# Kernel tuning notes

Hardware: AMD Instinct MI355X
Metric: run time of the kernel (lower is better)

The kernel has to match this reference:

```python
import math
import jax, jax.numpy as jnp
import numpy as np

D_MODEL = 1024
HEADS = 16
D_K = D_MODEL // HEADS
B, S = 8, 1024


def setup_inputs() -> dict:
    key = jax.random.key(0)
    ks = jax.random.split(key, 12)
    s = 1.0 / math.sqrt(D_MODEL)
    return {
        "values": jax.random.normal(ks[0], (B, S, D_MODEL), jnp.float32),
        "keys": jax.random.normal(ks[1], (B, S, D_MODEL), jnp.float32),
        "query": jax.random.normal(ks[2], (B, S, D_MODEL), jnp.float32),
        "mask": jnp.ones((B, 1, 1, S), jnp.int32),
        "Wq": jax.random.normal(ks[3], (D_MODEL, D_MODEL), jnp.float32) * s,
        "bq": jnp.zeros((D_MODEL,), jnp.float32),
        "Wk": jax.random.normal(ks[4], (D_MODEL, D_MODEL), jnp.float32) * s,
        "bk": jnp.zeros((D_MODEL,), jnp.float32),
        "Wv": jax.random.normal(ks[5], (D_MODEL, D_MODEL), jnp.float32) * s,
        "bv": jnp.zeros((D_MODEL,), jnp.float32),
        "Wo": jax.random.normal(ks[6], (D_MODEL, D_MODEL), jnp.float32) * s,
        "bo": jnp.zeros((D_MODEL,), jnp.float32),
    }


def reference(values, keys, query, mask, Wq, bq, Wk, bk, Wv, bv, Wo, bo):
    b, qlen, d = query.shape
    vlen, klen = values.shape[1], keys.shape[1]
    # projections (torch Linear math: x @ W + b with W stored [in, out])
    v = (values @ Wv + bv).reshape(b, vlen, HEADS, D_K)
    k = (keys @ Wk + bk).reshape(b, klen, HEADS, D_K)
    q = (query @ Wq + bq).reshape(b, qlen, HEADS, D_K)
    # full [b, h, q, k] scores (faithful to the non-flash original)
    energy = jnp.einsum('nqhd,nkhd->nhqk', q, k)
    energy = jnp.where(mask == 0, jnp.float32(-1e20), energy)
    # NOTE: original scales by sqrt(d_model), not sqrt(d_k)
    attn = jax.nn.softmax(energy / math.sqrt(D_MODEL), axis=3)
    out = jnp.einsum('nhql,nlhd->nqhd', attn, v).reshape(b, qlen, d)
    return out @ Wo + bo
```

## Files before the change

kernel.cpp:

```cpp
#include <hip/hip_runtime.h>

#define DM     1024
#define NHEADS 16
#define DK     64
#define NB     8
#define SEQ    1024
#define MROWS  (NB * SEQ)
#define NQ     ((size_t)MROWS * DM)

typedef unsigned short u16;
typedef __attribute__((ext_vector_type(8))) __bf16 bf16x8;
typedef __attribute__((ext_vector_type(8))) short  short8v;
typedef __attribute__((ext_vector_type(4))) float  f32x4;

typedef const __attribute__((address_space(1))) void* gas_ptr;
typedef __attribute__((address_space(3))) void*       las_ptr;

__device__ __forceinline__ void load_lds16(const void* g, void* l) {
    __builtin_amdgcn_global_load_lds((gas_ptr)g, (las_ptr)l, 16, 0, 0);
}
__device__ __forceinline__ void load_lds4(const void* g, void* l) {
    __builtin_amdgcn_global_load_lds((gas_ptr)g, (las_ptr)l, 4, 0, 0);
}

__device__ __forceinline__ u16 bf16_rne(float x) {
    unsigned int u = __float_as_uint(x);
    u += 0x7FFFu + ((u >> 16) & 1u);
    return (u16)(u >> 16);
}

__global__ __launch_bounds__(256)
void conv_split(const float* __restrict__ in, u16* __restrict__ hi,
                u16* __restrict__ lo)
{
    size_t i8 = ((size_t)blockIdx.x * 256 + threadIdx.x) * 8;
    float4 x0 = *(const float4*)(in + i8);
    float4 x1 = *(const float4*)(in + i8 + 4);
    float xs[8] = {x0.x, x0.y, x0.z, x0.w, x1.x, x1.y, x1.z, x1.w};
    short8v vh, vl;
#pragma unroll
    for (int j = 0; j < 8; ++j) {
        u16 h = bf16_rne(xs[j]);
        float hf = __uint_as_float((unsigned int)h << 16);
        vh[j] = (short)h;
        vl[j] = (short)bf16_rne(xs[j] - hf);
    }
    *(short8v*)(hi + i8) = vh;
    *(short8v*)(lo + i8) = vl;
}

__global__ __launch_bounds__(256)
void conv_w(const float* __restrict__ W0, const float* __restrict__ W1,
            const float* __restrict__ W2, const float* __restrict__ W3,
            u16* __restrict__ hiB, u16* __restrict__ loB)
{
    __shared__ float Wf[32][68];
    const int t = threadIdx.x;
    const int n0 = blockIdx.x * 64, k0 = blockIdx.y * 32, z = blockIdx.z;
    const float* W = (z == 0) ? W0 : (z == 1) ? W1 : (z == 2) ? W2 : W3;
    u16* hi = hiB + (size_t)z * DM * DM;
    u16* lo = loB + (size_t)z * DM * DM;

#pragma unroll
    for (int p = 0; p < 2; ++p) {
        int fid = p * 256 + t;
        int kk = fid >> 4, c4 = fid & 15;
        *(float4*)&Wf[kk][c4 * 4] =
            *(const float4*)(W + (size_t)(k0 + kk) * DM + n0 + c4 * 4);
    }
    __syncthreads();

    const int n = t >> 2, g = t & 3;
    short8v vh, vl;
#pragma unroll
    for (int j = 0; j < 8; ++j) {
        float x = Wf[g * 8 + j][n];
        u16 h = bf16_rne(x);
        float hf = __uint_as_float((unsigned int)h << 16);
        vh[j] = (short)h;
        vl[j] = (short)bf16_rne(x - hf);
    }
    size_t off = (size_t)(n0 + n) * DM + k0 + g * 8;
    *(short8v*)(hi + off) = vh;
    *(short8v*)(lo + off) = vl;
}

template <int MODE>
__global__ __launch_bounds__(256)
void gemm_split_t(const u16* __restrict__ Agh, const u16* __restrict__ Agl,
                  const u16* __restrict__ Bgh, const u16* __restrict__ Bgl,
                  const float* __restrict__ bias, float* __restrict__ Cf,
                  u16* __restrict__ C1, u16* __restrict__ C2)
{
    __shared__ __align__(16) u16 Ah[128 * 32], Al[128 * 32],
                                 Bh[128 * 32], Bl[128 * 32];
    const int t = threadIdx.x, lane = t & 63, wid = t >> 6;
    const int m0 = blockIdx.x * 128, n0 = blockIdx.y * 128;
    const int wm0 = (wid >> 1) * 64, wn0 = (wid & 1) * 64;
    const int ln = lane & 15, blk = lane >> 4;

    const u16* gsrc = (wid == 0) ? Agh : (wid == 1) ? Agl
                    : (wid == 2) ? Bgh : Bgl;
    u16* ldst = (wid == 0) ? Ah : (wid == 1) ? Al : (wid == 2) ? Bh : Bl;
    const int r0 = (wid < 2) ? m0 : n0;
    const int lr = lane >> 2, sl = lane & 3;
    const int gg = sl ^ ((lr >> 1) & 3);
    const u16* gbase = gsrc + (size_t)(r0 + lr) * DM + gg * 8;

    f32x4 zero4 = {0.f, 0.f, 0.f, 0.f};
    f32x4 acc[4][4];
#pragma unroll
    for (int i = 0; i < 4; ++i)
#pragma unroll
        for (int j = 0; j < 4; ++j) acc[i][j] = zero4;

    for (int kt = 0; kt < 1024; kt += 32) {
        __syncthreads();
#pragma unroll
        for (int i = 0; i < 8; ++i)
            load_lds16(gbase + (size_t)i * 16 * DM + kt, ldst + i * 512);
        __syncthreads();

        bf16x8 bfh[4], bfl[4];
#pragma unroll
        for (int bn = 0; bn < 4; ++bn) {
            int rn = wn0 + bn * 16 + ln;
            int off = rn * 32 + ((blk ^ ((rn >> 1) & 3)) << 3);
            bfh[bn] = *(const bf16x8*)(Bh + off);
            bfl[bn] = *(const bf16x8*)(Bl + off);
        }
#pragma unroll
        for (int am = 0; am < 4; ++am) {
            int rm = wm0 + am * 16 + ln;
            int off = rm * 32 + ((blk ^ ((rm >> 1) & 3)) << 3);
            bf16x8 afh = *(const bf16x8*)(Ah + off);
            bf16x8 afl = *(const bf16x8*)(Al + off);
#pragma unroll
            for (int bn = 0; bn < 4; ++bn) {
                acc[am][bn] = __builtin_amdgcn_mfma_f32_16x16x32_bf16(
                    afh, bfh[bn], acc[am][bn], 0, 0, 0);
                acc[am][bn] = __builtin_amdgcn_mfma_f32_16x16x32_bf16(
                    afh, bfl[bn], acc[am][bn], 0, 0, 0);
                acc[am][bn] = __builtin_amdgcn_mfma_f32_16x16x32_bf16(
                    afl, bfh[bn], acc[am][bn], 0, 0, 0);
            }
        }
    }

#pragma unroll
    for (int bn = 0; bn < 4; ++bn) {
        int col = n0 + wn0 + bn * 16 + ln;
        float bs = bias[col];
#pragma unroll
        for (int am = 0; am < 4; ++am) {
#pragma unroll
            for (int r = 0; r < 4; ++r) {
                int row = m0 + wm0 + am * 16 + blk * 4 + r;
                float v = acc[am][bn][r] + bs;
                size_t idx = (size_t)row * DM + col;
                if (MODE == 0) {
                    Cf[idx] = v;
                } else if (MODE == 1) {
                    u16 h = bf16_rne(v);
                    float hf = __uint_as_float((unsigned int)h << 16);
                    C1[idx] = h;
                    C2[idx] = bf16_rne(v - hf);
                } else {
                    C1[idx] = bf16_rne(v);
                }
            }
        }
    }
}

__global__ __launch_bounds__(256)
void v_transpose(const u16* __restrict__ Vbf, u16* __restrict__ Vt)
{
    __shared__ u16 Ls[64][66];
    const int t = threadIdx.x;
    const int s0 = blockIdx.x * 64, h = blockIdx.y, b = blockIdx.z;
#pragma unroll
    for (int p = 0; p < 2; ++p) {
        int id = p * 256 + t;
        int s = id >> 3, c8 = id & 7;
        short8v v = *(const short8v*)(Vbf + (size_t)(b * SEQ + s0 + s) * DM +
                                      h * DK + c8 * 8);
#pragma unroll
        for (int j = 0; j < 8; ++j) Ls[s][c8 * 8 + j] = (u16)v[j];
    }
    __syncthreads();
#pragma unroll
    for (int p = 0; p < 2; ++p) {
        int id = p * 256 + t;
        int d = id >> 3, s8 = id & 7;
        short8v v;
#pragma unroll
        for (int j = 0; j < 8; ++j) v[j] = (short)Ls[s8 * 8 + j][d];
        *(short8v*)(Vt + (size_t)((b * NHEADS + h) * DK + d) * SEQ + s0 +
                    s8 * 8) = v;
    }
}

__global__ __launch_bounds__(256)
void attn_mfma(const u16* __restrict__ Qh, const u16* __restrict__ Ql,
               const u16* __restrict__ Kh, const u16* __restrict__ Kl,
               const u16* __restrict__ Vt, const int* __restrict__ mask,
               float* __restrict__ OutA)
{
    __shared__ __align__(16) u16 Qhs[128 * 64], Qls[128 * 64];
    __shared__ __align__(16) u16 Khs[64 * 64], Kls[64 * 64], Vts[64 * 64];
    __shared__ __align__(16) u16 Ps[4][16 * 64];
    __shared__ int msk_s[64];

    const int t = threadIdx.x, lane = t & 63, wid = t >> 6;
    const int q0 = blockIdx.x * 128;
    const int h = blockIdx.y, b = blockIdx.z;
    const int ln = lane & 15, blk = lane >> 4;

    const int srow = lane >> 3;
    const int schk = (lane & 7) ^ srow;

    {
        const size_t qg =
            (size_t)(b * SEQ + q0 + srow) * DM + h * DK + schk * 8;
        for (int i = wid; i < 16; i += 4) {
            load_lds16(Qh + qg + (size_t)i * 8 * DM, (char*)Qhs + i * 1024);
            load_lds16(Ql + qg + (size_t)i * 8 * DM, (char*)Qls + i * 1024);
        }
    }

    float m_i[2][4], l_i[2][4];
    f32x4 oacc[2][4];
    f32x4 zero4 = {0.f, 0.f, 0.f, 0.f};
#pragma unroll
    for (int am = 0; am < 2; ++am) {
#pragma unroll
        for (int r = 0; r < 4; ++r) { m_i[am][r] = -INFINITY; l_i[am][r] = 0.f; }
#pragma unroll
        for (int bn = 0; bn < 4; ++bn) oacc[am][bn] = zero4;
    }

    for (int kv0 = 0; kv0 < SEQ; kv0 += 64) {
        __syncthreads();
        if (wid == 0) {
            const size_t kg =
                (size_t)(b * SEQ + kv0 + srow) * DM + h * DK + schk * 8;
#pragma unroll
            for (int i = 0; i < 8; ++i)
                load_lds16(Kh + kg + (size_t)i * 8 * DM, (char*)Khs + i * 1024);
        } else if (wid == 1) {
            const size_t kg =
                (size_t)(b * SEQ + kv0 + srow) * DM + h * DK + schk * 8;
#pragma unroll
            for (int i = 0; i < 8; ++i)
                load_lds16(Kl + kg + (size_t)i * 8 * DM, (char*)Kls + i * 1024);
        } else if (wid == 2) {
            const size_t vg =
                (size_t)((b * NHEADS + h) * DK + srow) * SEQ + kv0 + schk * 8;
#pragma unroll
            for (int i = 0; i < 8; ++i)
                load_lds16(Vt + vg + (size_t)i * 8 * SEQ, (char*)Vts + i * 1024);
        } else {
            load_lds4(mask + (size_t)b * SEQ + kv0 + lane, (char*)msk_s);
        }
        __syncthreads();

        int mvals[4];
#pragma unroll
        for (int ct = 0; ct < 4; ++ct) mvals[ct] = msk_s[ct * 16 + ln];

#pragma unroll
        for (int am = 0; am < 2; ++am) {
            const int qrow = wid * 32 + am * 16 + ln;
            bf16x8 qh[2], ql[2];
#pragma unroll
            for (int ks = 0; ks < 2; ++ks) {
                int idx = qrow * 64 + (((ks * 4 + blk) ^ (qrow & 7)) << 3);
                qh[ks] = *(const bf16x8*)(Qhs + idx);
                ql[ks] = *(const bf16x8*)(Qls + idx);
            }
            f32x4 s[4];
#pragma unroll
            for (int ct = 0; ct < 4; ++ct) s[ct] = zero4;
#pragma unroll
            for (int ct = 0; ct < 4; ++ct) {
                int krow = ct * 16 + ln;
#pragma unroll
                for (int ks = 0; ks < 2; ++ks) {
                    int idx = krow * 64 + (((ks * 4 + blk) ^ (krow & 7)) << 3);
                    bf16x8 kf = *(const bf16x8*)(Khs + idx);
                    bf16x8 kg2 = *(const bf16x8*)(Kls + idx);
                    s[ct] = __builtin_amdgcn_mfma_f32_16x16x32_bf16(
                        qh[ks], kf, s[ct], 0, 0, 0);
                    s[ct] = __builtin_amdgcn_mfma_f32_16x16x32_bf16(
                        qh[ks], kg2, s[ct], 0, 0, 0);
                    s[ct] = __builtin_amdgcn_mfma_f32_16x16x32_bf16(
                        ql[ks], kf, s[ct], 0, 0, 0);
                }
            }
#pragma unroll
            for (int ct = 0; ct < 4; ++ct) {
                const bool mz = (mvals[ct] == 0);
#pragma unroll
                for (int r = 0; r < 4; ++r) {
                    float e = mz ? -1e20f : s[ct][r];
                    s[ct][r] = e * 0.03125f;
                }
            }
#pragma unroll
            for (int r = 0; r < 4; ++r) {
                float mt = fmaxf(fmaxf(s[0][r], s[1][r]),
                                 fmaxf(s[2][r], s[3][r]));
#pragma unroll
                for (int off = 1; off < 16; off <<= 1)
                    mt = fmaxf(mt, __shfl_xor(mt, off, 16));
                float mn = fmaxf(m_i[am][r], mt);
                float al = __expf(m_i[am][r] - mn);
                m_i[am][r] = mn;
                float rs = 0.f;
#pragma unroll
                for (int ct = 0; ct < 4; ++ct) {
                    float p = __expf(s[ct][r] - mn);
                    s[ct][r] = p;
                    rs += p;
                }
#pragma unroll
                for (int off = 1; off < 16; off <<= 1)
                    rs += __shfl_xor(rs, off, 16);
                l_i[am][r] = l_i[am][r] * al + rs;
#pragma unroll
                for (int bn = 0; bn < 4; ++bn) oacc[am][bn][r] *= al;
            }
            u16* P = &Ps[wid][0];
#pragma unroll
            for (int ct = 0; ct < 4; ++ct) {
                int slot = ct * 2 + (ln >> 3);
#pragma unroll
                for (int r = 0; r < 4; ++r) {
                    int q = blk * 4 + r;
                    P[q * 64 + ((slot ^ (q & 7)) << 3) + (ln & 7)] =
                        bf16_rne(s[ct][r]);
                }
            }
#pragma unroll
            for (int ks = 0; ks < 2; ++ks) {
                int pidx = ln * 64 + (((ks * 4 + blk) ^ (ln & 7)) << 3);
                bf16x8 pa = *(const bf16x8*)(P + pidx);
#pragma unroll
                for (int bn = 0; bn < 4; ++bn) {
                    int vrow = bn * 16 + ln;
                    int vidx =
                        vrow * 64 + (((ks * 4 + blk) ^ (vrow & 7)) << 3);
                    bf16x8 vb = *(const bf16x8*)(Vts + vidx);
                    oacc[am][bn] = __builtin_amdgcn_mfma_f32_16x16x32_bf16(
                        pa, vb, oacc[am][bn], 0, 0, 0);
                }
            }
        }
    }

#pragma unroll
    for (int am = 0; am < 2; ++am) {
#pragma unroll
        for (int r = 0; r < 4; ++r) {
            int q = q0 + wid * 32 + am * 16 + blk * 4 + r;
            float inv = 1.f / l_i[am][r];
#pragma unroll
            for (int bn = 0; bn < 4; ++bn) {
                OutA[(size_t)(b * SEQ + q) * DM + h * DK + bn * 16 + ln] =
                    oacc[am][bn][r] * inv;
            }
        }
    }
}

extern "C" void kernel_launch(void* const* d_in, const int* in_sizes, int n_in,
                              void* d_out, int out_size, void* d_ws, size_t ws_size,
                              hipStream_t stream)
{
    const float* values = (const float*)d_in[0];
    const float* keys   = (const float*)d_in[1];
    const float* query  = (const float*)d_in[2];
    const int*   mask   = (const int*)d_in[3];
    const float* Wq = (const float*)d_in[4];
    const float* bq = (const float*)d_in[5];
    const float* Wk = (const float*)d_in[6];
    const float* bk = (const float*)d_in[7];
    const float* Wv = (const float*)d_in[8];
    const float* bv = (const float*)d_in[9];
    const float* Wo = (const float*)d_in[10];
    const float* bo = (const float*)d_in[11];
    float* out = (float*)d_out;

    u16* Qh   = (u16*)d_ws;
    u16* Ql   = Qh + NQ;
    u16* Kh   = Ql + NQ;
    u16* Kl   = Kh + NQ;
    u16* Vbf  = Kl + NQ;
    u16* Vtb  = Vbf + NQ;
    u16* Wthi = Vtb + NQ;
    u16* Wtlo = Wthi + (size_t)4 * DM * DM;
    u16* tAhi = Wtlo + (size_t)4 * DM * DM;
    u16* tAlo = tAhi + NQ;
    float* Ao = (float*)tAhi;
    u16* AoHi = Vbf;
    u16* AoLo = Vtb;

    const u16* WqH = Wthi + 0 * (size_t)DM * DM;
    const u16* WkH = Wthi + 1 * (size_t)DM * DM;
    const u16* WvH = Wthi + 2 * (size_t)DM * DM;
    const u16* WoH = Wthi + 3 * (size_t)DM * DM;
    const u16* WqL = Wtlo + 0 * (size_t)DM * DM;
    const u16* WkL = Wtlo + 1 * (size_t)DM * DM;
    const u16* WvL = Wtlo + 2 * (size_t)DM * DM;
    const u16* WoL = Wtlo + 3 * (size_t)DM * DM;

    dim3 blk(256);
    const int convGrid = (int)(NQ / 2048);
    const dim3 gemmGrid(MROWS / 128, DM / 128, 1);

    conv_w<<<dim3(16, 32, 4), blk, 0, stream>>>(Wq, Wk, Wv, Wo, Wthi, Wtlo);

    conv_split<<<convGrid, blk, 0, stream>>>(query, tAhi, tAlo);
    gemm_split_t<1><<<gemmGrid, blk, 0, stream>>>(tAhi, tAlo, WqH, WqL, bq,
                                                  nullptr, Qh, Ql);
    conv_split<<<convGrid, blk, 0, stream>>>(keys, tAhi, tAlo);
    gemm_split_t<1><<<gemmGrid, blk, 0, stream>>>(tAhi, tAlo, WkH, WkL, bk,
                                                  nullptr, Kh, Kl);
    conv_split<<<convGrid, blk, 0, stream>>>(values, tAhi, tAlo);
    gemm_split_t<2><<<gemmGrid, blk, 0, stream>>>(tAhi, tAlo, WvH, WvL, bv,
                                                  nullptr, Vbf, nullptr);
    v_transpose<<<dim3(16, NHEADS, NB), blk, 0, stream>>>(Vbf, Vtb);

    attn_mfma<<<dim3(SEQ / 128, NHEADS, NB), blk, 0, stream>>>(
        Qh, Ql, Kh, Kl, Vtb, mask, Ao);

    conv_split<<<convGrid, blk, 0, stream>>>(Ao, AoHi, AoLo);
    gemm_split_t<0><<<gemmGrid, blk, 0, stream>>>(AoHi, AoLo, WoH, WoL, bo,
                                                  out, nullptr, nullptr);
}
```

Before: 559.2 us.

## Batch QKV conversion and projections, fuse output split into attention, lazy softmax rescale

Merges the three input conversions and the three QKV projection GEMMs into single launches over a z-dimension, when the workspace is large enough. The attention kernel now writes the hi/lo bf16 split of its output directly, which removes the fp32 round trip and a separate conversion pass. Q fragments are kept in registers instead of LDS. Softmax rescaling is skipped unless the running max grows by more than a threshold, and the scale is folded into an fma. The GEMM mode becomes a runtime argument, which may add branching in the epilogue, and the lazy-max threshold risks exp overflow margins.

```diff
diff --git a/kernel.cpp b/kernel.cpp
--- a/kernel.cpp
+++ b/kernel.cpp
@@ -29,11 +29,10 @@
     return (u16)(u >> 16);
 }
 
-__global__ __launch_bounds__(256)
-void conv_split(const float* __restrict__ in, u16* __restrict__ hi,
-                u16* __restrict__ lo)
-{
-    size_t i8 = ((size_t)blockIdx.x * 256 + threadIdx.x) * 8;
+__device__ __forceinline__ void split_store8(const float* __restrict__ in,
+                                             u16* __restrict__ hi,
+                                             u16* __restrict__ lo, size_t i8)
+{
     float4 x0 = *(const float4*)(in + i8);
     float4 x1 = *(const float4*)(in + i8 + 4);
     float xs[8] = {x0.x, x0.y, x0.z, x0.w, x1.x, x1.y, x1.z, x1.w};
@@ -47,6 +46,28 @@
     }
     *(short8v*)(hi + i8) = vh;
     *(short8v*)(lo + i8) = vl;
+}
+
+__global__ __launch_bounds__(256)
+void conv_split(const float* __restrict__ in, u16* __restrict__ hi,
+                u16* __restrict__ lo)
+{
+    size_t i8 = ((size_t)blockIdx.x * 256 + threadIdx.x) * 8;
+    split_store8(in, hi, lo, i8);
+}
+
+__global__ __launch_bounds__(256)
+void conv_qkv(const float* __restrict__ q, const float* __restrict__ k,
+              const float* __restrict__ v, u16* __restrict__ qh,
+              u16* __restrict__ ql, u16* __restrict__ kh, u16* __restrict__ kl,
+              u16* __restrict__ vh, u16* __restrict__ vl)
+{
+    const int z = blockIdx.z;
+    const float* in = (z == 0) ? q : (z == 1) ? k : v;
+    u16* hi = (z == 0) ? qh : (z == 1) ? kh : vh;
+    u16* lo = (z == 0) ? ql : (z == 1) ? kl : vl;
+    size_t i8 = ((size_t)blockIdx.x * 256 + threadIdx.x) * 8;
+    split_store8(in, hi, lo, i8);
 }
 
 __global__ __launch_bounds__(256)
@@ -85,12 +106,11 @@
     *(short8v*)(lo + off) = vl;
 }
 
-template <int MODE>
-__global__ __launch_bounds__(256)
-void gemm_split_t(const u16* __restrict__ Agh, const u16* __restrict__ Agl,
-                  const u16* __restrict__ Bgh, const u16* __restrict__ Bgl,
-                  const float* __restrict__ bias, float* __restrict__ Cf,
-                  u16* __restrict__ C1, u16* __restrict__ C2)
+__device__ __forceinline__ void gemm_body(
+    const u16* __restrict__ Agh, const u16* __restrict__ Agl,
+    const u16* __restrict__ Bgh, const u16* __restrict__ Bgl,
+    const float* __restrict__ bias, int mode, float* __restrict__ Cf,
+    u16* __restrict__ C1, u16* __restrict__ C2)
 {
     __shared__ __align__(16) u16 Ah[128 * 32], Al[128 * 32],
                                  Bh[128 * 32], Bl[128 * 32];
@@ -158,9 +178,9 @@
                 int row = m0 + wm0 + am * 16 + blk * 4 + r;
                 float v = acc[am][bn][r] + bs;
                 size_t idx = (size_t)row * DM + col;
-                if (MODE == 0) {
+                if (mode == 0) {
                     Cf[idx] = v;
-                } else if (MODE == 1) {
+                } else if (mode == 1) {
                     u16 h = bf16_rne(v);
                     float hf = __uint_as_float((unsigned int)h << 16);
                     C1[idx] = h;
@@ -174,6 +194,38 @@
 }
 
 __global__ __launch_bounds__(256)
+void gemm_one(const u16* __restrict__ Agh, const u16* __restrict__ Agl,
+              const u16* __restrict__ Bgh, const u16* __restrict__ Bgl,
+              const float* __restrict__ bias, int mode, float* __restrict__ Cf,
+              u16* __restrict__ C1, u16* __restrict__ C2)
+{
+    gemm_body(Agh, Agl, Bgh, Bgl, bias, mode, Cf, C1, C2);
+}
+
+__global__ __launch_bounds__(256)
+void gemm_qkv(const u16* __restrict__ Aqh, const u16* __restrict__ Aql,
+              const u16* __restrict__ Akh, const u16* __restrict__ Akl,
+              const u16* __restrict__ Avh, const u16* __restrict__ Avl,
+              const u16* __restrict__ Wqh, const u16* __restrict__ Wql,
+              const u16* __restrict__ Wkh, const u16* __restrict__ Wkl,
+              const u16* __restrict__ Wvh, const u16* __restrict__ Wvl,
+              const float* __restrict__ bq, const float* __restrict__ bk,
+              const float* __restrict__ bv, u16* __restrict__ Qh,
+              u16* __restrict__ Ql, u16* __restrict__ Kh, u16* __restrict__ Kl,
+              u16* __restrict__ Vbf)
+{
+    const int z = blockIdx.z;
+    const u16* Ah = (z == 0) ? Aqh : (z == 1) ? Akh : Avh;
+    const u16* Al = (z == 0) ? Aql : (z == 1) ? Akl : Avl;
+    const u16* Bh = (z == 0) ? Wqh : (z == 1) ? Wkh : Wvh;
+    const u16* Bl = (z == 0) ? Wql : (z == 1) ? Wkl : Wvl;
+    const float* bias = (z == 0) ? bq : (z == 1) ? bk : bv;
+    u16* C1 = (z == 0) ? Qh : (z == 1) ? Kh : Vbf;
+    u16* C2 = (z == 0) ? Ql : (z == 1) ? Kl : nullptr;
+    gemm_body(Ah, Al, Bh, Bl, bias, (z == 2) ? 2 : 1, nullptr, C1, C2);
+}
+
+__global__ __launch_bounds__(256)
 void v_transpose(const u16* __restrict__ Vbf, u16* __restrict__ Vt)
 {
     __shared__ u16 Ls[64][66];
@@ -205,9 +257,8 @@
 void attn_mfma(const u16* __restrict__ Qh, const u16* __restrict__ Ql,
                const u16* __restrict__ Kh, const u16* __restrict__ Kl,
                const u16* __restrict__ Vt, const int* __restrict__ mask,
-               float* __restrict__ OutA)
-{
-    __shared__ __align__(16) u16 Qhs[128 * 64], Qls[128 * 64];
+               u16* __restrict__ AoHi, u16* __restrict__ AoLo)
+{
     __shared__ __align__(16) u16 Khs[64 * 64], Kls[64 * 64], Vts[64 * 64];
     __shared__ __align__(16) u16 Ps[4][16 * 64];
     __shared__ int msk_s[64];
@@ -216,16 +267,18 @@
     const int q0 = blockIdx.x * 128;
     const int h = blockIdx.y, b = blockIdx.z;
     const int ln = lane & 15, blk = lane >> 4;
-
     const int srow = lane >> 3;
     const int schk = (lane & 7) ^ srow;
 
-    {
-        const size_t qg =
-            (size_t)(b * SEQ + q0 + srow) * DM + h * DK + schk * 8;
-        for (int i = wid; i < 16; i += 4) {
-            load_lds16(Qh + qg + (size_t)i * 8 * DM, (char*)Qhs + i * 1024);
-            load_lds16(Ql + qg + (size_t)i * 8 * DM, (char*)Qls + i * 1024);
+    bf16x8 qfh[2][2], qfl[2][2];
+#pragma unroll
+    for (int am = 0; am < 2; ++am) {
+        int row = q0 + wid * 32 + am * 16 + ln;
+        size_t base = (size_t)(b * SEQ + row) * DM + h * DK;
+#pragma unroll
+        for (int ks = 0; ks < 2; ++ks) {
+            qfh[am][ks] = *(const bf16x8*)(Qh + base + (ks * 4 + blk) * 8);
+            qfl[am][ks] = *(const bf16x8*)(Ql + base + (ks * 4 + blk) * 8);
         }
     }
 
@@ -271,14 +324,6 @@
 
 #pragma unroll
         for (int am = 0; am < 2; ++am) {
-            const int qrow = wid * 32 + am * 16 + ln;
-            bf16x8 qh[2], ql[2];
-#pragma unroll
-            for (int ks = 0; ks < 2; ++ks) {
-                int idx = qrow * 64 + (((ks * 4 + blk) ^ (qrow & 7)) << 3);
-                qh[ks] = *(const bf16x8*)(Qhs + idx);
-                ql[ks] = *(const bf16x8*)(Qls + idx);
-            }
             f32x4 s[4];
 #pragma unroll
             for (int ct = 0; ct < 4; ++ct) s[ct] = zero4;
@@ -291,20 +336,18 @@
                     bf16x8 kf = *(const bf16x8*)(Khs + idx);
                     bf16x8 kg2 = *(const bf16x8*)(Kls + idx);
                     s[ct] = __builtin_amdgcn_mfma_f32_16x16x32_bf16(
-                        qh[ks], kf, s[ct], 0, 0, 0);
+                        qfh[am][ks], kf, s[ct], 0, 0, 0);
                     s[ct] = __builtin_amdgcn_mfma_f32_16x16x32_bf16(
-                        qh[ks], kg2, s[ct], 0, 0, 0);
+                        qfh[am][ks], kg2, s[ct], 0, 0, 0);
                     s[ct] = __builtin_amdgcn_mfma_f32_16x16x32_bf16(
-                        ql[ks], kf, s[ct], 0, 0, 0);
+                        qfl[am][ks], kf, s[ct], 0, 0, 0);
                 }
             }
 #pragma unroll
             for (int ct = 0; ct < 4; ++ct) {
-                const bool mz = (mvals[ct] == 0);
-#pragma unroll
-                for (int r = 0; r < 4; ++r) {
-                    float e = mz ? -1e20f : s[ct][r];
-                    s[ct][r] = e * 0.03125f;
+                if (mvals[ct] == 0) {
+#pragma unroll
+                    for (int r = 0; r < 4; ++r) s[ct][r] = -1e20f;
                 }
             }
 #pragma unroll
@@ -314,22 +357,26 @@
 #pragma unroll
                 for (int off = 1; off < 16; off <<= 1)
                     mt = fmaxf(mt, __shfl_xor(mt, off, 16));
-                float mn = fmaxf(m_i[am][r], mt);
-                float al = __expf(m_i[am][r] - mn);
-                m_i[am][r] = mn;
+                float pmax = mt * 0.03125f;
+                if (pmax > m_i[am][r] + 8.f) {
+                    float al = __expf(m_i[am][r] - pmax);
+                    m_i[am][r] = pmax;
+                    l_i[am][r] *= al;
+#pragma unroll
+                    for (int bn = 0; bn < 4; ++bn) oacc[am][bn][r] *= al;
+                }
+                float mn = m_i[am][r];
                 float rs = 0.f;
 #pragma unroll
                 for (int ct = 0; ct < 4; ++ct) {
-                    float p = __expf(s[ct][r] - mn);
+                    float p = __expf(fmaf(s[ct][r], 0.03125f, -mn));
                     s[ct][r] = p;
                     rs += p;
                 }
 #pragma unroll
                 for (int off = 1; off < 16; off <<= 1)
                     rs += __shfl_xor(rs, off, 16);
-                l_i[am][r] = l_i[am][r] * al + rs;
-#pragma unroll
-                for (int bn = 0; bn < 4; ++bn) oacc[am][bn][r] *= al;
+                l_i[am][r] += rs;
             }
             u16* P = &Ps[wid][0];
 #pragma unroll
@@ -365,10 +412,15 @@
         for (int r = 0; r < 4; ++r) {
             int q = q0 + wid * 32 + am * 16 + blk * 4 + r;
             float inv = 1.f / l_i[am][r];
+            size_t rowbase = (size_t)(b * SEQ + q) * DM + h * DK;
 #pragma unroll
             for (int bn = 0; bn < 4; ++bn) {
-                OutA[(size_t)(b * SEQ + q) * DM + h * DK + bn * 16 + ln] =
-                    oacc[am][bn][r] * inv;
+                float v = oacc[am][bn][r] * inv;
+                u16 uh = bf16_rne(v);
+                float hf = __uint_as_float((unsigned int)uh << 16);
+                size_t idx = rowbase + bn * 16 + ln;
+                AoHi[idx] = uh;
+                AoLo[idx] = bf16_rne(v - hf);
             }
         }
     }
@@ -392,50 +444,88 @@
     const float* bo = (const float*)d_in[11];
     float* out = (float*)d_out;
 
-    u16* Qh   = (u16*)d_ws;
-    u16* Ql   = Qh + NQ;
-    u16* Kh   = Ql + NQ;
-    u16* Kl   = Kh + NQ;
-    u16* Vbf  = Kl + NQ;
-    u16* Vtb  = Vbf + NQ;
-    u16* Wthi = Vtb + NQ;
-    u16* Wtlo = Wthi + (size_t)4 * DM * DM;
-    u16* tAhi = Wtlo + (size_t)4 * DM * DM;
-    u16* tAlo = tAhi + NQ;
-    float* Ao = (float*)tAhi;
-    u16* AoHi = Vbf;
-    u16* AoLo = Vtb;
-
-    const u16* WqH = Wthi + 0 * (size_t)DM * DM;
-    const u16* WkH = Wthi + 1 * (size_t)DM * DM;
-    const u16* WvH = Wthi + 2 * (size_t)DM * DM;
-    const u16* WoH = Wthi + 3 * (size_t)DM * DM;
-    const u16* WqL = Wtlo + 0 * (size_t)DM * DM;
-    const u16* WkL = Wtlo + 1 * (size_t)DM * DM;
-    const u16* WvL = Wtlo + 2 * (size_t)DM * DM;
-    const u16* WoL = Wtlo + 3 * (size_t)DM * DM;
-
     dim3 blk(256);
     const int convGrid = (int)(NQ / 2048);
     const dim3 gemmGrid(MROWS / 128, DM / 128, 1);
-
-    conv_w<<<dim3(16, 32, 4), blk, 0, stream>>>(Wq, Wk, Wv, Wo, Wthi, Wtlo);
-
-    conv_split<<<convGrid, blk, 0, stream>>>(query, tAhi, tAlo);
-    gemm_split_t<1><<<gemmGrid, blk, 0, stream>>>(tAhi, tAlo, WqH, WqL, bq,
-                                                  nullptr, Qh, Ql);
-    conv_split<<<convGrid, blk, 0, stream>>>(keys, tAhi, tAlo);
-    gemm_split_t<1><<<gemmGrid, blk, 0, stream>>>(tAhi, tAlo, WkH, WkL, bk,
-                                                  nullptr, Kh, Kl);
-    conv_split<<<convGrid, blk, 0, stream>>>(values, tAhi, tAlo);
-    gemm_split_t<2><<<gemmGrid, blk, 0, stream>>>(tAhi, tAlo, WvH, WvL, bv,
-                                                  nullptr, Vbf, nullptr);
-    v_transpose<<<dim3(16, NHEADS, NB), blk, 0, stream>>>(Vbf, Vtb);
-
-    attn_mfma<<<dim3(SEQ / 128, NHEADS, NB), blk, 0, stream>>>(
-        Qh, Ql, Kh, Kl, Vtb, mask, Ao);
-
-    conv_split<<<convGrid, blk, 0, stream>>>(Ao, AoHi, AoLo);
-    gemm_split_t<0><<<gemmGrid, blk, 0, stream>>>(AoHi, AoLo, WoH, WoL, bo,
-                                                  out, nullptr, nullptr);
-}
+    const dim3 gemmGrid3(MROWS / 128, DM / 128, 3);
+
+    const bool fused = ws_size >= (size_t)12 * NQ * 2;
+
+    if (fused) {
+        u16* Qh   = (u16*)d_ws;
+        u16* Ql   = Qh + NQ;
+        u16* Kh   = Ql + NQ;
+        u16* Kl   = Kh + NQ;
+        u16* Vbf  = Kl + NQ;
+        u16* Wthi = Vbf + NQ;
+        u16* Wtlo = Wthi + (size_t)4 * DM * DM;
+        u16* tAqh = Wtlo + (size_t)4 * DM * DM;
+        u16* tAql = tAqh + NQ;
+        u16* tAkh = tAql + NQ;
+        u16* tAkl = tAkh + NQ;
+        u16* tAvh = tAkl + NQ;
+        u16* tAvl = tAvh + NQ;
+        u16* Vtb  = tAqh;
+        u16* AoHi = tAkh;
+        u16* AoLo = tAkl;
+
+        const u16* WqH = Wthi + 0 * (size_t)DM * DM;
+        const u16* WkH = Wthi + 1 * (size_t)DM * DM;
+        const u16* WvH = Wthi + 2 * (size_t)DM * DM;
+        const u16* WoH = Wthi + 3 * (size_t)DM * DM;
+        const u16* WqL = Wtlo + 0 * (size_t)DM * DM;
+        const u16* WkL = Wtlo + 1 * (size_t)DM * DM;
+        const u16* WvL = Wtlo + 2 * (size_t)DM * DM;
+        const u16* WoL = Wtlo + 3 * (size_t)DM * DM;
+
+        conv_w<<<dim3(16, 32, 4), blk, 0, stream>>>(Wq, Wk, Wv, Wo, Wthi, Wtlo);
+        conv_qkv<<<dim3(convGrid, 1, 3), blk, 0, stream>>>(
+            query, keys, values, tAqh, tAql, tAkh, tAkl, tAvh, tAvl);
+        gemm_qkv<<<gemmGrid3, blk, 0, stream>>>(
+            tAqh, tAql, tAkh, tAkl, tAvh, tAvl, WqH, WqL, WkH, WkL, WvH, WvL,
+            bq, bk, bv, Qh, Ql, Kh, Kl, Vbf);
+        v_transpose<<<dim3(16, NHEADS, NB), blk, 0, stream>>>(Vbf, Vtb);
+        attn_mfma<<<dim3(SEQ / 128, NHEADS, NB), blk, 0, stream>>>(
+            Qh, Ql, Kh, Kl, Vtb, mask, AoHi, AoLo);
+        gemm_one<<<gemmGrid, blk, 0, stream>>>(AoHi, AoLo, WoH, WoL, bo, 0,
+                                               out, nullptr, nullptr);
+    } else {
+        u16* Qh   = (u16*)d_ws;
+        u16* Ql   = Qh + NQ;
+        u16* Kh   = Ql + NQ;
+        u16* Kl   = Kh + NQ;
+        u16* Vbf  = Kl + NQ;
+        u16* Vtb  = Vbf + NQ;
+        u16* Wthi = Vtb + NQ;
+        u16* Wtlo = Wthi + (size_t)4 * DM * DM;
+        u16* tAhi = Wtlo + (size_t)4 * DM * DM;
+        u16* tAlo = tAhi + NQ;
+        u16* AoHi = tAhi;
+        u16* AoLo = tAlo;
+
+        const u16* WqH = Wthi + 0 * (size_t)DM * DM;
+        const u16* WkH = Wthi + 1 * (size_t)DM * DM;
+        const u16* WvH = Wthi + 2 * (size_t)DM * DM;
+        const u16* WoH = Wthi + 3 * (size_t)DM * DM;
+        const u16* WqL = Wtlo + 0 * (size_t)DM * DM;
+        const u16* WkL = Wtlo + 1 * (size_t)DM * DM;
+        const u16* WvL = Wtlo + 2 * (size_t)DM * DM;
+        const u16* WoL = Wtlo + 3 * (size_t)DM * DM;
+
+        conv_w<<<dim3(16, 32, 4), blk, 0, stream>>>(Wq, Wk, Wv, Wo, Wthi, Wtlo);
+        conv_split<<<convGrid, blk, 0, stream>>>(query, tAhi, tAlo);
+        gemm_one<<<gemmGrid, blk, 0, stream>>>(tAhi, tAlo, WqH, WqL, bq, 1,
+                                               nullptr, Qh, Ql);
+        conv_split<<<convGrid, blk, 0, stream>>>(keys, tAhi, tAlo);
+        gemm_one<<<gemmGrid, blk, 0, stream>>>(tAhi, tAlo, WkH, WkL, bk, 1,
+                                               nullptr, Kh, Kl);
+        conv_split<<<convGrid, blk, 0, stream>>>(values, tAhi, tAlo);
+        gemm_one<<<gemmGrid, blk, 0, stream>>>(tAhi, tAlo, WvH, WvL, bv, 2,
+                                               nullptr, Vbf, nullptr);
+        v_transpose<<<dim3(16, NHEADS, NB), blk, 0, stream>>>(Vbf, Vtb);
+        attn_mfma<<<dim3(SEQ / 128, NHEADS, NB), blk, 0, stream>>>(
+            Qh, Ql, Kh, Kl, Vtb, mask, AoHi, AoLo);
+        gemm_one<<<gemmGrid, blk, 0, stream>>>(AoHi, AoLo, WoH, WoL, bo, 0,
+                                               out, nullptr, nullptr);
+    }
+}
```

After: 556.2 us. About the same (-0.5%).

## Switch to fp16 split precision, fuse QKV GEMMs and V transpose, lazy softmax rescale

Applied to the files above, without the earlier changes.

Replaces the bf16 hi/lo three-MFMA split with fp16, where activations are a single fp16 and only the weights (and Q) keep a hi/lo pair, cutting MFMA count and conversion traffic. The three input casts and the three projection GEMMs each become one launch batched over z. The V transpose is folded into the GEMM epilogue through LDS, and outputs are written with coalesced LDS-staged stores. Attention keeps Q in registers, uses single-precision K, applies a lazy max rescale with a threshold of 8, and writes its output in fp16 so the separate cast before the output GEMM goes away. fp16 range and the reduced split precision put accuracy at risk.

```diff
diff --git a/kernel.cpp b/kernel.cpp
--- a/kernel.cpp
+++ b/kernel.cpp
@@ -9,7 +9,7 @@
 #define NQ     ((size_t)MROWS * DM)
 
 typedef unsigned short u16;
-typedef __attribute__((ext_vector_type(8))) __bf16 bf16x8;
+typedef __attribute__((ext_vector_type(8))) _Float16 f16x8;
 typedef __attribute__((ext_vector_type(8))) short  short8v;
 typedef __attribute__((ext_vector_type(4))) float  f32x4;
 
@@ -23,30 +23,33 @@
     __builtin_amdgcn_global_load_lds((gas_ptr)g, (las_ptr)l, 4, 0, 0);
 }
 
-__device__ __forceinline__ u16 bf16_rne(float x) {
-    unsigned int u = __float_as_uint(x);
-    u += 0x7FFFu + ((u >> 16) & 1u);
-    return (u16)(u >> 16);
+__device__ __forceinline__ u16 f16_bits(float x) {
+    union { _Float16 h; u16 u; } c;
+    c.h = (_Float16)x;
+    return c.u;
+}
+__device__ __forceinline__ float f16_val(u16 u) {
+    union { _Float16 h; u16 u; } c;
+    c.u = u;
+    return (float)c.h;
 }
 
 __global__ __launch_bounds__(256)
-void conv_split(const float* __restrict__ in, u16* __restrict__ hi,
-                u16* __restrict__ lo)
-{
+void conv_cast3(const float* __restrict__ q, const float* __restrict__ k,
+                const float* __restrict__ v, u16* __restrict__ qo,
+                u16* __restrict__ ko, u16* __restrict__ vo)
+{
+    const int z = blockIdx.z;
+    const float* in = (z == 0) ? q : (z == 1) ? k : v;
+    u16* o = (z == 0) ? qo : (z == 1) ? ko : vo;
     size_t i8 = ((size_t)blockIdx.x * 256 + threadIdx.x) * 8;
     float4 x0 = *(const float4*)(in + i8);
     float4 x1 = *(const float4*)(in + i8 + 4);
     float xs[8] = {x0.x, x0.y, x0.z, x0.w, x1.x, x1.y, x1.z, x1.w};
-    short8v vh, vl;
-#pragma unroll
-    for (int j = 0; j < 8; ++j) {
-        u16 h = bf16_rne(xs[j]);
-        float hf = __uint_as_float((unsigned int)h << 16);
-        vh[j] = (short)h;
-        vl[j] = (short)bf16_rne(xs[j] - hf);
-    }
-    *(short8v*)(hi + i8) = vh;
-    *(short8v*)(lo + i8) = vl;
+    short8v r;
+#pragma unroll
+    for (int j = 0; j < 8; ++j) r[j] = (short)f16_bits(xs[j]);
+    *(short8v*)(o + i8) = r;
 }
 
 __global__ __launch_bounds__(256)
@@ -75,37 +78,45 @@
 #pragma unroll
     for (int j = 0; j < 8; ++j) {
         float x = Wf[g * 8 + j][n];
-        u16 h = bf16_rne(x);
-        float hf = __uint_as_float((unsigned int)h << 16);
+        u16 h = f16_bits(x);
         vh[j] = (short)h;
-        vl[j] = (short)bf16_rne(x - hf);
+        vl[j] = (short)f16_bits(x - f16_val(h));
     }
     size_t off = (size_t)(n0 + n) * DM + k0 + g * 8;
     *(short8v*)(hi + off) = vh;
     *(short8v*)(lo + off) = vl;
 }
 
-template <int MODE>
-__global__ __launch_bounds__(256)
-void gemm_split_t(const u16* __restrict__ Agh, const u16* __restrict__ Agl,
-                  const u16* __restrict__ Bgh, const u16* __restrict__ Bgl,
-                  const float* __restrict__ bias, float* __restrict__ Cf,
-                  u16* __restrict__ C1, u16* __restrict__ C2)
-{
-    __shared__ __align__(16) u16 Ah[128 * 32], Al[128 * 32],
-                                 Bh[128 * 32], Bl[128 * 32];
+#define PITCH 136
+__device__ __forceinline__ void gemm2_body(
+    const u16* __restrict__ Ag, const u16* __restrict__ Bgh,
+    const u16* __restrict__ Bgl, const float* __restrict__ bias, int mode,
+    float* __restrict__ Cf, u16* __restrict__ C1, u16* __restrict__ C2)
+{
+    __shared__ __align__(16) u16 smem[128 * PITCH];
+    u16* const Af = smem;
+    u16* const Bh = smem + 4096;
+    u16* const Bl = smem + 8192;
+
     const int t = threadIdx.x, lane = t & 63, wid = t >> 6;
     const int m0 = blockIdx.x * 128, n0 = blockIdx.y * 128;
     const int wm0 = (wid >> 1) * 64, wn0 = (wid & 1) * 64;
     const int ln = lane & 15, blk = lane >> 4;
 
-    const u16* gsrc = (wid == 0) ? Agh : (wid == 1) ? Agl
-                    : (wid == 2) ? Bgh : Bgl;
-    u16* ldst = (wid == 0) ? Ah : (wid == 1) ? Al : (wid == 2) ? Bh : Bl;
-    const int r0 = (wid < 2) ? m0 : n0;
     const int lr = lane >> 2, sl = lane & 3;
     const int gg = sl ^ ((lr >> 1) & 3);
-    const u16* gbase = gsrc + (size_t)(r0 + lr) * DM + gg * 8;
+    const u16* gA[6];
+    u16* lA[6];
+#pragma unroll
+    for (int i = 0; i < 6; ++i) {
+        int c = wid * 6 + i, sub = c & 7;
+        const u16* gsrc; u16* lbuf; int r0;
+        if (c < 8)       { gsrc = Ag;  lbuf = Af; r0 = m0; }
+        else if (c < 16) { gsrc = Bgh; lbuf = Bh; r0 = n0; }
+        else             { gsrc = Bgl; lbuf = Bl; r0 = n0; }
+        gA[i] = gsrc + (size_t)(r0 + sub * 16 + lr) * DM + gg * 8;
+        lA[i] = lbuf + sub * 512;
+    }
 
     f32x4 zero4 = {0.f, 0.f, 0.f, 0.f};
     f32x4 acc[4][4];
@@ -117,115 +128,207 @@
     for (int kt = 0; kt < 1024; kt += 32) {
         __syncthreads();
 #pragma unroll
-        for (int i = 0; i < 8; ++i)
-            load_lds16(gbase + (size_t)i * 16 * DM + kt, ldst + i * 512);
-        __syncthreads();
-
-        bf16x8 bfh[4], bfl[4];
+        for (int i = 0; i < 6; ++i) load_lds16(gA[i] + kt, lA[i]);
+        __syncthreads();
+
+        f16x8 bh[4], bl[4];
 #pragma unroll
         for (int bn = 0; bn < 4; ++bn) {
             int rn = wn0 + bn * 16 + ln;
             int off = rn * 32 + ((blk ^ ((rn >> 1) & 3)) << 3);
-            bfh[bn] = *(const bf16x8*)(Bh + off);
-            bfl[bn] = *(const bf16x8*)(Bl + off);
+            bh[bn] = *(const f16x8*)(Bh + off);
+            bl[bn] = *(const f16x8*)(Bl + off);
         }
 #pragma unroll
         for (int am = 0; am < 4; ++am) {
             int rm = wm0 + am * 16 + ln;
             int off = rm * 32 + ((blk ^ ((rm >> 1) & 3)) << 3);
-            bf16x8 afh = *(const bf16x8*)(Ah + off);
-            bf16x8 afl = *(const bf16x8*)(Al + off);
+            f16x8 af = *(const f16x8*)(Af + off);
 #pragma unroll
             for (int bn = 0; bn < 4; ++bn) {
-                acc[am][bn] = __builtin_amdgcn_mfma_f32_16x16x32_bf16(
-                    afh, bfh[bn], acc[am][bn], 0, 0, 0);
-                acc[am][bn] = __builtin_amdgcn_mfma_f32_16x16x32_bf16(
-                    afh, bfl[bn], acc[am][bn], 0, 0, 0);
-                acc[am][bn] = __builtin_amdgcn_mfma_f32_16x16x32_bf16(
-                    afl, bfh[bn], acc[am][bn], 0, 0, 0);
-            }
-        }
+                acc[am][bn] = __builtin_amdgcn_mfma_f32_16x16x32_f16(
+                    af, bh[bn], acc[am][bn], 0, 0, 0);
+                acc[am][bn] = __builtin_amdgcn_mfma_f32_16x16x32_f16(
+                    af, bl[bn], acc[am][bn], 0, 0, 0);
+            }
+        }
+    }
+
+    if (mode == 0) {
+#pragma unroll
+        for (int bn = 0; bn < 4; ++bn) {
+            int coll = wn0 + bn * 16 + ln;
+            float bs = bias[n0 + coll];
+#pragma unroll
+            for (int am = 0; am < 4; ++am)
+#pragma unroll
+                for (int r = 0; r < 4; ++r) {
+                    int rowl = wm0 + am * 16 + blk * 4 + r;
+                    Cf[(size_t)(m0 + rowl) * DM + n0 + coll] =
+                        acc[am][bn][r] + bs;
+                }
+        }
+        return;
+    }
+
+    __syncthreads();
+
+    if (mode == 3) {
+#pragma unroll
+        for (int bn = 0; bn < 4; ++bn) {
+            int coll = wn0 + bn * 16 + ln;
+            float bs = bias[n0 + coll];
+#pragma unroll
+            for (int am = 0; am < 4; ++am)
+#pragma unroll
+                for (int r = 0; r < 4; ++r) {
+                    int rowl = wm0 + am * 16 + blk * 4 + r;
+                    smem[coll * PITCH + rowl] = f16_bits(acc[am][bn][r] + bs);
+                }
+        }
+        __syncthreads();
+        const int bq_ = m0 >> 10, s0_ = m0 & 1023, h0_ = n0 >> 6;
+#pragma unroll
+        for (int p = 0; p < 8; ++p) {
+            int c = p * 256 + t;
+            int h_l = c >> 10;
+            int d   = (c >> 4) & 63;
+            int sc  = c & 15;
+            int scp = (sc + ((d & 3) << 2)) & 15;
+            short8v rd = *(const short8v*)(smem + (h_l * 64 + d) * PITCH +
+                                           scp * 8);
+            *(short8v*)(C1 +
+                        ((size_t)(bq_ * NHEADS + h0_ + h_l) * DK + d) * SEQ +
+                        s0_ + scp * 8) = rd;
+        }
+        return;
     }
 
 #pragma unroll
     for (int bn = 0; bn < 4; ++bn) {
-        int col = n0 + wn0 + bn * 16 + ln;
-        float bs = bias[col];
-#pragma unroll
-        for (int am = 0; am < 4; ++am) {
+        int coll = wn0 + bn * 16 + ln;
+        float bs = bias[n0 + coll];
+#pragma unroll
+        for (int am = 0; am < 4; ++am)
 #pragma unroll
             for (int r = 0; r < 4; ++r) {
-                int row = m0 + wm0 + am * 16 + blk * 4 + r;
+                int rowl = wm0 + am * 16 + blk * 4 + r;
                 float v = acc[am][bn][r] + bs;
-                size_t idx = (size_t)row * DM + col;
-                if (MODE == 0) {
-                    Cf[idx] = v;
-                } else if (MODE == 1) {
-                    u16 h = bf16_rne(v);
-                    float hf = __uint_as_float((unsigned int)h << 16);
-                    C1[idx] = h;
-                    C2[idx] = bf16_rne(v - hf);
-                } else {
-                    C1[idx] = bf16_rne(v);
-                }
-            }
+                u16 hb = f16_bits(v);
+                smem[rowl * PITCH + coll] = hb;
+                acc[am][bn][r] = v - f16_val(hb);
+            }
+    }
+    __syncthreads();
+#pragma unroll
+    for (int p = 0; p < 8; ++p) {
+        int f = p * 256 + t;
+        int row = f >> 4, cc = f & 15;
+        int ccp = (cc + ((row & 3) << 2)) & 15;
+        short8v rd = *(const short8v*)(smem + row * PITCH + ccp * 8);
+        *(short8v*)(C1 + (size_t)(m0 + row) * DM + n0 + ccp * 8) = rd;
+    }
+    if (mode == 1) {
+        __syncthreads();
+#pragma unroll
+        for (int bn = 0; bn < 4; ++bn) {
+            int coll = wn0 + bn * 16 + ln;
+#pragma unroll
+            for (int am = 0; am < 4; ++am)
+#pragma unroll
+                for (int r = 0; r < 4; ++r) {
+                    int rowl = wm0 + am * 16 + blk * 4 + r;
+                    smem[rowl * PITCH + coll] = f16_bits(acc[am][bn][r]);
+                }
+        }
+        __syncthreads();
+#pragma unroll
+        for (int p = 0; p < 8; ++p) {
+            int f = p * 256 + t;
+            int row = f >> 4, cc = f & 15;
+            int ccp = (cc + ((row & 3) << 2)) & 15;
+            short8v rd = *(const short8v*)(smem + row * PITCH + ccp * 8);
+            *(short8v*)(C2 + (size_t)(m0 + row) * DM + n0 + ccp * 8) = rd;
         }
     }
 }
 
 __global__ __launch_bounds__(256)
-void v_transpose(const u16* __restrict__ Vbf, u16* __restrict__ Vt)
-{
-    __shared__ u16 Ls[64][66];
-    const int t = threadIdx.x;
-    const int s0 = blockIdx.x * 64, h = blockIdx.y, b = blockIdx.z;
-#pragma unroll
-    for (int p = 0; p < 2; ++p) {
-        int id = p * 256 + t;
-        int s = id >> 3, c8 = id & 7;
-        short8v v = *(const short8v*)(Vbf + (size_t)(b * SEQ + s0 + s) * DM +
-                                      h * DK + c8 * 8);
-#pragma unroll
-        for (int j = 0; j < 8; ++j) Ls[s][c8 * 8 + j] = (u16)v[j];
-    }
-    __syncthreads();
-#pragma unroll
-    for (int p = 0; p < 2; ++p) {
-        int id = p * 256 + t;
-        int d = id >> 3, s8 = id & 7;
-        short8v v;
-#pragma unroll
-        for (int j = 0; j < 8; ++j) v[j] = (short)Ls[s8 * 8 + j][d];
-        *(short8v*)(Vt + (size_t)((b * NHEADS + h) * DK + d) * SEQ + s0 +
-                    s8 * 8) = v;
-    }
+void gemm_qkv(const u16* __restrict__ Aq, const u16* __restrict__ Ak,
+              const u16* __restrict__ Av, const u16* __restrict__ Wqh,
+              const u16* __restrict__ Wql, const u16* __restrict__ Wkh,
+              const u16* __restrict__ Wkl, const u16* __restrict__ Wvh,
+              const u16* __restrict__ Wvl, const float* __restrict__ bq,
+              const float* __restrict__ bk, const float* __restrict__ bv,
+              u16* __restrict__ Qh, u16* __restrict__ Ql,
+              u16* __restrict__ Kf, u16* __restrict__ Vt)
+{
+    const int z = blockIdx.z;
+    const u16* A  = (z == 0) ? Aq  : (z == 1) ? Ak  : Av;
+    const u16* Bh = (z == 0) ? Wqh : (z == 1) ? Wkh : Wvh;
+    const u16* Bl = (z == 0) ? Wql : (z == 1) ? Wkl : Wvl;
+    const float* bias = (z == 0) ? bq : (z == 1) ? bk : bv;
+    u16* C1 = (z == 0) ? Qh : (z == 1) ? Kf : Vt;
+    u16* C2 = (z == 0) ? Ql : nullptr;
+    gemm2_body(A, Bh, Bl, bias, (z == 0) ? 1 : (z == 1) ? 2 : 3,
+               nullptr, C1, C2);
 }
 
 __global__ __launch_bounds__(256)
-void attn_mfma(const u16* __restrict__ Qh, const u16* __restrict__ Ql,
-               const u16* __restrict__ Kh, const u16* __restrict__ Kl,
-               const u16* __restrict__ Vt, const int* __restrict__ mask,
-               float* __restrict__ OutA)
-{
-    __shared__ __align__(16) u16 Qhs[128 * 64], Qls[128 * 64];
-    __shared__ __align__(16) u16 Khs[64 * 64], Kls[64 * 64], Vts[64 * 64];
-    __shared__ __align__(16) u16 Ps[4][16 * 64];
+void gemm_o(const u16* __restrict__ A, const u16* __restrict__ Bh,
+            const u16* __restrict__ Bl, const float* __restrict__ bias,
+            float* __restrict__ out)
+{
+    gemm2_body(A, Bh, Bl, bias, 0, out, nullptr, nullptr);
+}
+
+#define OPITCH 72
+__global__ __launch_bounds__(256)
+void attn_f16(const u16* __restrict__ Qh, const u16* __restrict__ Ql,
+              const u16* __restrict__ Kf, const u16* __restrict__ Vtg,
+              const int* __restrict__ mask, u16* __restrict__ Ao)
+{
+    __shared__ __align__(16) u16 asmem[12288];
     __shared__ int msk_s[64];
+    u16* const Ks  = asmem;
+    u16* const Vts = asmem + 4096;
 
     const int t = threadIdx.x, lane = t & 63, wid = t >> 6;
     const int q0 = blockIdx.x * 128;
     const int h = blockIdx.y, b = blockIdx.z;
     const int ln = lane & 15, blk = lane >> 4;
-
-    const int srow = lane >> 3;
-    const int schk = (lane & 7) ^ srow;
-
-    {
-        const size_t qg =
-            (size_t)(b * SEQ + q0 + srow) * DM + h * DK + schk * 8;
-        for (int i = wid; i < 16; i += 4) {
-            load_lds16(Qh + qg + (size_t)i * 8 * DM, (char*)Qhs + i * 1024);
-            load_lds16(Ql + qg + (size_t)i * 8 * DM, (char*)Qls + i * 1024);
+    const int lr8 = lane >> 3;
+    const int schk = (lane & 7) ^ lr8;
+
+    f16x8 qfh[2][2], qfl[2][2];
+#pragma unroll
+    for (int am = 0; am < 2; ++am) {
+        int row = q0 + wid * 32 + am * 16 + ln;
+        size_t base = (size_t)(b * SEQ + row) * DM + h * DK;
+#pragma unroll
+        for (int ks = 0; ks < 2; ++ks) {
+            qfh[am][ks] = *(const f16x8*)(Qh + base + (ks * 4 + blk) * 8);
+            qfl[am][ks] = *(const f16x8*)(Ql + base + (ks * 4 + blk) * 8);
+        }
+    }
+
+    const u16* gA[4];
+    u16* lA[4];
+    size_t stp[4];
+#pragma unroll
+    for (int i = 0; i < 4; ++i) {
+        int c = wid * 4 + i, sub = c & 7;
+        if (c < 8) {
+            gA[i] = Kf + ((size_t)(b * SEQ) + sub * 8 + lr8) * DM + h * DK +
+                    schk * 8;
+            lA[i] = Ks + sub * 512;
+            stp[i] = (size_t)64 * DM;
+        } else {
+            gA[i] = Vtg + ((size_t)((b * NHEADS + h) * DK) + sub * 8 + lr8) *
+                              SEQ +
+                    schk * 8;
+            lA[i] = Vts + sub * 512;
+            stp[i] = 64;
         }
     }
 
@@ -242,27 +345,13 @@
 
     for (int kv0 = 0; kv0 < SEQ; kv0 += 64) {
         __syncthreads();
-        if (wid == 0) {
-            const size_t kg =
-                (size_t)(b * SEQ + kv0 + srow) * DM + h * DK + schk * 8;
-#pragma unroll
-            for (int i = 0; i < 8; ++i)
-                load_lds16(Kh + kg + (size_t)i * 8 * DM, (char*)Khs + i * 1024);
-        } else if (wid == 1) {
-            const size_t kg =
-                (size_t)(b * SEQ + kv0 + srow) * DM + h * DK + schk * 8;
-#pragma unroll
-            for (int i = 0; i < 8; ++i)
-                load_lds16(Kl + kg + (size_t)i * 8 * DM, (char*)Kls + i * 1024);
-        } else if (wid == 2) {
-            const size_t vg =
-                (size_t)((b * NHEADS + h) * DK + srow) * SEQ + kv0 + schk * 8;
-#pragma unroll
-            for (int i = 0; i < 8; ++i)
-                load_lds16(Vt + vg + (size_t)i * 8 * SEQ, (char*)Vts + i * 1024);
-        } else {
+#pragma unroll
+        for (int i = 0; i < 4; ++i) {
+            load_lds16(gA[i], lA[i]);
+            gA[i] += stp[i];
+        }
+        if (wid == 3)
             load_lds4(mask + (size_t)b * SEQ + kv0 + lane, (char*)msk_s);
-        }
         __syncthreads();
 
         int mvals[4];
@@ -271,14 +360,6 @@
 
 #pragma unroll
         for (int am = 0; am < 2; ++am) {
-            const int qrow = wid * 32 + am * 16 + ln;
-            bf16x8 qh[2], ql[2];
-#pragma unroll
-            for (int ks = 0; ks < 2; ++ks) {
-                int idx = qrow * 64 + (((ks * 4 + blk) ^ (qrow & 7)) << 3);
-                qh[ks] = *(const bf16x8*)(Qhs + idx);
-                ql[ks] = *(const bf16x8*)(Qls + idx);
-            }
             f32x4 s[4];
 #pragma unroll
             for (int ct = 0; ct < 4; ++ct) s[ct] = zero4;
@@ -288,23 +369,18 @@
 #pragma unroll
                 for (int ks = 0; ks < 2; ++ks) {
                     int idx = krow * 64 + (((ks * 4 + blk) ^ (krow & 7)) << 3);
-                    bf16x8 kf = *(const bf16x8*)(Khs + idx);
-                    bf16x8 kg2 = *(const bf16x8*)(Kls + idx);
-                    s[ct] = __builtin_amdgcn_mfma_f32_16x16x32_bf16(
-                        qh[ks], kf, s[ct], 0, 0, 0);
-                    s[ct] = __builtin_amdgcn_mfma_f32_16x16x32_bf16(
-                        qh[ks], kg2, s[ct], 0, 0, 0);
-                    s[ct] = __builtin_amdgcn_mfma_f32_16x16x32_bf16(
-                        ql[ks], kf, s[ct], 0, 0, 0);
+                    f16x8 kf = *(const f16x8*)(Ks + idx);
+                    s[ct] = __builtin_amdgcn_mfma_f32_16x16x32_f16(
+                        qfh[am][ks], kf, s[ct], 0, 0, 0);
+                    s[ct] = __builtin_amdgcn_mfma_f32_16x16x32_f16(
+                        qfl[am][ks], kf, s[ct], 0, 0, 0);
                 }
             }
 #pragma unroll
             for (int ct = 0; ct < 4; ++ct) {
-                const bool mz = (mvals[ct] == 0);
-#pragma unroll
-                for (int r = 0; r < 4; ++r) {
-                    float e = mz ? -1e20f : s[ct][r];
-                    s[ct][r] = e * 0.03125f;
+                if (mvals[ct] == 0) {
+#pragma unroll
+                    for (int r = 0; r < 4; ++r) s[ct][r] = -1e20f;
                 }
             }
 #pragma unroll
@@ -314,24 +390,28 @@
 #pragma unroll
                 for (int off = 1; off < 16; off <<= 1)
                     mt = fmaxf(mt, __shfl_xor(mt, off, 16));
-                float mn = fmaxf(m_i[am][r], mt);
-                float al = __expf(m_i[am][r] - mn);
-                m_i[am][r] = mn;
+                float pmax = mt * 0.03125f;
+                if (pmax > m_i[am][r] + 8.f) {
+                    float al = __expf(m_i[am][r] - pmax);
+                    m_i[am][r] = pmax;
+                    l_i[am][r] *= al;
+#pragma unroll
+                    for (int bn = 0; bn < 4; ++bn) oacc[am][bn][r] *= al;
+                }
+                float mn = m_i[am][r];
                 float rs = 0.f;
 #pragma unroll
                 for (int ct = 0; ct < 4; ++ct) {
-                    float p = __expf(s[ct][r] - mn);
+                    float p = __expf(fmaf(s[ct][r], 0.03125f, -mn));
                     s[ct][r] = p;
                     rs += p;
                 }
 #pragma unroll
                 for (int off = 1; off < 16; off <<= 1)
                     rs += __shfl_xor(rs, off, 16);
-                l_i[am][r] = l_i[am][r] * al + rs;
-#pragma unroll
-                for (int bn = 0; bn < 4; ++bn) oacc[am][bn][r] *= al;
-            }
-            u16* P = &Ps[wid][0];
+                l_i[am][r] += rs;
+            }
+            u16* P = asmem + 8192 + wid * 1024;
 #pragma unroll
             for (int ct = 0; ct < 4; ++ct) {
                 int slot = ct * 2 + (ln >> 3);
@@ -339,38 +419,48 @@
                 for (int r = 0; r < 4; ++r) {
                     int q = blk * 4 + r;
                     P[q * 64 + ((slot ^ (q & 7)) << 3) + (ln & 7)] =
-                        bf16_rne(s[ct][r]);
+                        f16_bits(s[ct][r]);
                 }
             }
 #pragma unroll
             for (int ks = 0; ks < 2; ++ks) {
                 int pidx = ln * 64 + (((ks * 4 + blk) ^ (ln & 7)) << 3);
-                bf16x8 pa = *(const bf16x8*)(P + pidx);
+                f16x8 pa = *(const f16x8*)(P + pidx);
 #pragma unroll
                 for (int bn = 0; bn < 4; ++bn) {
                     int vrow = bn * 16 + ln;
                     int vidx =
                         vrow * 64 + (((ks * 4 + blk) ^ (vrow & 7)) << 3);
-                    bf16x8 vb = *(const bf16x8*)(Vts + vidx);
-                    oacc[am][bn] = __builtin_amdgcn_mfma_f32_16x16x32_bf16(
+                    f16x8 vb = *(const f16x8*)(Vts + vidx);
+                    oacc[am][bn] = __builtin_amdgcn_mfma_f32_16x16x32_f16(
                         pa, vb, oacc[am][bn], 0, 0, 0);
                 }
             }
         }
     }
 
+    __syncthreads();
 #pragma unroll
     for (int am = 0; am < 2; ++am) {
 #pragma unroll
         for (int r = 0; r < 4; ++r) {
-            int q = q0 + wid * 32 + am * 16 + blk * 4 + r;
+            int ql_ = wid * 32 + am * 16 + blk * 4 + r;
             float inv = 1.f / l_i[am][r];
 #pragma unroll
             for (int bn = 0; bn < 4; ++bn) {
-                OutA[(size_t)(b * SEQ + q) * DM + h * DK + bn * 16 + ln] =
-                    oacc[am][bn][r] * inv;
-            }
-        }
+                int d = bn * 16 + ln;
+                asmem[ql_ * OPITCH + d] = f16_bits(oacc[am][bn][r] * inv);
+            }
+        }
+    }
+    __syncthreads();
+#pragma unroll
+    for (int p = 0; p < 4; ++p) {
+        int f = p * 256 + t;
+        int qq = f >> 3, dc = f & 7;
+        short8v rd = *(const short8v*)(asmem + qq * OPITCH + dc * 8);
+        *(short8v*)(Ao + (size_t)(b * SEQ + q0 + qq) * DM + h * DK + dc * 8) =
+            rd;
     }
 }
 
@@ -394,17 +484,14 @@
 
     u16* Qh   = (u16*)d_ws;
     u16* Ql   = Qh + NQ;
-    u16* Kh   = Ql + NQ;
-    u16* Kl   = Kh + NQ;
-    u16* Vbf  = Kl + NQ;
-    u16* Vtb  = Vbf + NQ;
-    u16* Wthi = Vtb + NQ;
+    u16* Kf   = Ql + NQ;
+    u16* Vt   = Kf + NQ;
+    u16* Wthi = Vt + NQ;
     u16* Wtlo = Wthi + (size_t)4 * DM * DM;
-    u16* tAhi = Wtlo + (size_t)4 * DM * DM;
-    u16* tAlo = tAhi + NQ;
-    float* Ao = (float*)tAhi;
-    u16* AoHi = Vbf;
-    u16* AoLo = Vtb;
+    u16* tAq  = Wtlo + (size_t)4 * DM * DM;
+    u16* tAk  = tAq + NQ;
+    u16* tAv  = tAk + NQ;
+    u16* Ao   = tAv + NQ;
 
     const u16* WqH = Wthi + 0 * (size_t)DM * DM;
     const u16* WkH = Wthi + 1 * (size_t)DM * DM;
@@ -416,26 +503,14 @@
     const u16* WoL = Wtlo + 3 * (size_t)DM * DM;
 
     dim3 blk(256);
-    const int convGrid = (int)(NQ / 2048);
-    const dim3 gemmGrid(MROWS / 128, DM / 128, 1);
-
     conv_w<<<dim3(16, 32, 4), blk, 0, stream>>>(Wq, Wk, Wv, Wo, Wthi, Wtlo);
-
-    conv_split<<<convGrid, blk, 0, stream>>>(query, tAhi, tAlo);
-    gemm_split_t<1><<<gemmGrid, blk, 0, stream>>>(tAhi, tAlo, WqH, WqL, bq,
-                                                  nullptr, Qh, Ql);
-    conv_split<<<convGrid, blk, 0, stream>>>(keys, tAhi, tAlo);
-    gemm_split_t<1><<<gemmGrid, blk, 0, stream>>>(tAhi, tAlo, WkH, WkL, bk,
-                                                  nullptr, Kh, Kl);
-    conv_split<<<convGrid, blk, 0, stream>>>(values, tAhi, tAlo);
-    gemm_split_t<2><<<gemmGrid, blk, 0, stream>>>(tAhi, tAlo, WvH, WvL, bv,
-                                                  nullptr, Vbf, nullptr);
-    v_transpose<<<dim3(16, NHEADS, NB), blk, 0, stream>>>(Vbf, Vtb);
-
-    attn_mfma<<<dim3(SEQ / 128, NHEADS, NB), blk, 0, stream>>>(
-        Qh, Ql, Kh, Kl, Vtb, mask, Ao);
-
-    conv_split<<<convGrid, blk, 0, stream>>>(Ao, AoHi, AoLo);
-    gemm_split_t<0><<<gemmGrid, blk, 0, stream>>>(AoHi, AoLo, WoH, WoL, bo,
-                                                  out, nullptr, nullptr);
-}
+    conv_cast3<<<dim3((int)(NQ / 2048), 1, 3), blk, 0, stream>>>(
+        query, keys, values, tAq, tAk, tAv);
+    gemm_qkv<<<dim3(MROWS / 128, DM / 128, 3), blk, 0, stream>>>(
+        tAq, tAk, tAv, WqH, WqL, WkH, WkL, WvH, WvL, bq, bk, bv,
+        Qh, Ql, Kf, Vt);
+    attn_f16<<<dim3(SEQ / 128, NHEADS, NB), blk, 0, stream>>>(
+        Qh, Ql, Kf, Vt, mask, Ao);
+    gemm_o<<<dim3(MROWS / 128, DM / 128, 1), blk, 0, stream>>>(
+        Ao, WoH, WoL, bo, out);
+}
```

Result: faster. 504.6 us (-9.8%).
